# Performance work log

Measured on AMD Instinct MI355X. Metric: run time of the kernel, lower is better.

## Reference

```python
import jax, jax.numpy as jnp
import numpy as np

BN_EPS = 1e-5
R = 8.0        # radius
L = 11         # sequence kernel size (odd), s = L//2
K = 24         # kernel_channels[-1]
N_NODES = 32768
N_EDGES = 524288
C_IN = 128     # in_channels == out_channels
C_W = 32       # width = out_channels * base_width / 64


def _bn(x, gamma, beta):
    # BatchNorm1d in training mode: biased batch statistics over node dim
    mu = jnp.mean(x, axis=0)
    var = jnp.mean(jnp.square(x - mu), axis=0)
    return (x - mu) * jax.lax.rsqrt(var + BN_EPS) * gamma + beta


def _lrelu(x, slope):
    return jnp.where(x >= 0, x, slope * x)


def setup_inputs() -> dict:
    key = jax.random.key(0)
    ks = jax.random.split(key, 10)

    def glorot(k, shape, fan_in):
        return jax.random.normal(k, shape, jnp.float32) * np.float32(1.0 / np.sqrt(fan_in))

    inp = {}
    inp["x"] = jax.random.normal(ks[0], (N_NODES, C_IN), jnp.float32)
    inp["pos"] = jax.random.normal(ks[1], (N_NODES, 3), jnp.float32) * 10.0
    inp["ori"] = jax.random.normal(ks[2], (N_NODES, 9), jnp.float32)
    inp["seq"] = jnp.arange(N_NODES, dtype=jnp.int32)
    inp["edge_index"] = jax.random.randint(ks[3], (2, N_EDGES), 0, N_NODES, jnp.int32)
    # input MLP params: BN(C_IN) -> LeakyReLU(0.1) -> Linear(C_IN->C_W, no bias) -> BN(C_W) -> LeakyReLU(0.1)
    inp["bn1_g"] = jnp.ones((C_IN,), jnp.float32)
    inp["bn1_b"] = jnp.zeros((C_IN,), jnp.float32)
    inp["lin1_w"] = glorot(ks[4], (C_IN, C_W), C_IN)
    inp["bn2_g"] = jnp.ones((C_W,), jnp.float32)
    inp["bn2_b"] = jnp.zeros((C_W,), jnp.float32)
    # CDConv WeightNet (single layer kernel_channels=[K]): per-seq-bin affine 7 -> K
    inp["wn_w"] = glorot(ks[5], (L, 7, K), 7)
    inp["wn_b"] = jnp.zeros((L, K), jnp.float32)
    # CDConv output projection: [K*C_W, C_W]
    inp["conv_w"] = glorot(ks[6], (K * C_W, C_W), K * C_W)
    # output Linear: BN(C_W) -> LeakyReLU(0.1) -> Linear(C_W->C_IN, no bias)
    inp["bn3_g"] = jnp.ones((C_W,), jnp.float32)
    inp["bn3_b"] = jnp.zeros((C_W,), jnp.float32)
    inp["lin2_w"] = glorot(ks[7], (C_W, C_IN), C_W)
    return inp


def reference(x, pos, ori, seq, edge_index,
              bn1_g, bn1_b, lin1_w, bn2_g, bn2_b,
              wn_w, wn_b, conv_w, bn3_g, bn3_b, lin2_w):
    n = x.shape[0]
    identity = x  # in_channels == out_channels -> identity branch is passthrough

    # ----- input MLP (mid_channels=None) -----
    h = _lrelu(_bn(x, bn1_g, bn1_b), 0.1)
    h = h @ lin1_w                       # [N, C_W]
    h = _lrelu(_bn(h, bn2_g, bn2_b), 0.1)

    # ----- CDConv: continuous geometric kernel over neighbor edges -----
    src, dst = edge_index[0], edge_index[1]      # message j=src -> i=dst
    d = pos[src] - pos[dst]                      # [E,3]
    dist = jnp.linalg.norm(d, axis=-1, keepdims=True)
    direction = d / (dist + 1e-9)
    Ri = ori[dst].reshape(-1, 3, 3)              # receiver local frame
    Rj = ori[src].reshape(-1, 3, 3)
    pos_local = jnp.einsum('eij,ej->ei', Ri, direction)      # direction in local frame
    ori_feat = jnp.einsum('eij,ej->ei', Ri, Rj[:, 0, :])     # neighbor axis in local frame
    delta = jnp.concatenate([pos_local, ori_feat, dist / R], axis=-1)  # [E,7]

    s = L // 2
    sidx = jnp.clip(seq[src] - seq[dst], -s, s) + s          # [E] in [0, L)

    # WeightNet: per-edge affine selected by sequence bin, LeakyReLU(0.2)
    w = _lrelu(jnp.einsum('ef,efk->ek', delta, wn_w[sidx]) + wn_b[sidx], 0.2)  # [E,K]

    # message = outer(kernel_weight, x_j), scatter-sum to receivers
    msg = (w[:, :, None] * h[src][:, None, :]).reshape(w.shape[0], K * C_W)   # [E, K*C_W]
    agg = jax.ops.segment_sum(msg, dst, num_segments=n)                        # [N, K*C_W]
    h = agg @ conv_w                                                            # [N, C_W]

    # ----- output Linear + residual -----
    h = _lrelu(_bn(h, bn3_g, bn3_b), 0.1)
    out = h @ lin2_w + identity
    return out
```

## Files before the change

kernel.cpp:

```cpp
#include <hip/hip_runtime.h>

#define N_NODES 32768
#define C_IN 128
#define C_W 32
#define KK 24
#define SS 5
#define NPB 4
#define TC 256
#define AGS (KK * C_W + 4)
#define WNS 172
#define WBS 28
#define HS 36

#define BF_LO(u) __uint_as_float((u) << 16)
#define BF_HI(u) __uint_as_float((u) & 0xFFFF0000u)

__device__ __forceinline__ unsigned int bf16pair(float lo, float hi) {
    unsigned int ulo = __float_as_uint(lo);
    unsigned int uhi = __float_as_uint(hi);
    ulo = (ulo + 0x7FFFu + ((ulo >> 16) & 1u)) >> 16;
    uhi = (uhi + 0x7FFFu + ((uhi >> 16) & 1u)) & 0xFFFF0000u;
    return uhi | ulo;
}

__global__ void __launch_bounds__(256) k_pre(
        const float* __restrict__ x, float* __restrict__ s1,
        const int* __restrict__ ei, int E, int* __restrict__ counts) {
    int t = threadIdx.x;
    int c = t % C_IN;
    int r0 = blockIdx.x * 2 + t / C_IN;
    float s = 0.f, sq = 0.f;
    for (int r = r0; r < N_NODES; r += 1024) {
        float v = x[(size_t)r * C_IN + c];
        s += v; sq += v * v;
    }
    atomicAdd(&s1[c], s);
    atomicAdd(&s1[C_IN + c], sq);
    for (int e = blockIdx.x * 256 + t; e < E; e += 512 * 256)
        atomicAdd(&counts[ei[E + e]], 1);
}

__global__ void __launch_bounds__(256) k_mlp1(
        const float* __restrict__ x, const float* __restrict__ s1,
        const float* __restrict__ g1, const float* __restrict__ b1,
        const float* __restrict__ w1, float* __restrict__ hpre,
        float* __restrict__ s2sh) {
    __shared__ float sAB[2][C_IN];
    __shared__ float sx[32][C_IN + 4];
    __shared__ float sw[C_IN][C_W];
    const int t = threadIdx.x;
    const int row0 = blockIdx.x * 32;
    if (t < C_IN) {
        float mean = s1[t] * (1.f / N_NODES);
        float var = s1[C_IN + t] * (1.f / N_NODES) - mean * mean;
        float a = g1[t] * rsqrtf(var + 1e-5f);
        sAB[0][t] = a; sAB[1][t] = b1[t] - mean * a;
    }
    for (int idx = t; idx < C_IN * C_W; idx += 256)
        sw[idx / C_W][idx % C_W] = w1[idx];
    __syncthreads();
    for (int idx = t; idx < 32 * 32; idx += 256) {
        int r = idx >> 5, cq = idx & 31;
        float4 v = *(const float4*)&x[(size_t)(row0 + r) * C_IN + cq * 4];
        float* d = &sx[r][cq * 4];
        float a0 = sAB[0][cq*4+0]*v.x + sAB[1][cq*4+0];
        float a1 = sAB[0][cq*4+1]*v.y + sAB[1][cq*4+1];
        float a2 = sAB[0][cq*4+2]*v.z + sAB[1][cq*4+2];
        float a3 = sAB[0][cq*4+3]*v.w + sAB[1][cq*4+3];
        d[0] = a0 >= 0.f ? a0 : 0.1f * a0;
        d[1] = a1 >= 0.f ? a1 : 0.1f * a1;
        d[2] = a2 >= 0.f ? a2 : 0.1f * a2;
        d[3] = a3 >= 0.f ? a3 : 0.1f * a3;
    }
    __syncthreads();
    const int r = t >> 3, c0 = (t & 7) * 4;
    float ac0 = 0.f, ac1 = 0.f, ac2 = 0.f, ac3 = 0.f;
    #pragma unroll 8
    for (int cc = 0; cc < C_IN; ++cc) {
        float xv = sx[r][cc];
        float4 wv = *(const float4*)&sw[cc][c0];
        ac0 += xv * wv.x; ac1 += xv * wv.y; ac2 += xv * wv.z; ac3 += xv * wv.w;
    }
    float4 o; o.x = ac0; o.y = ac1; o.z = ac2; o.w = ac3;
    *(float4*)&hpre[(size_t)(row0 + r) * C_W + c0] = o;
    __syncthreads();
    sx[r][c0] = ac0; sx[r][c0+1] = ac1; sx[r][c0+2] = ac2; sx[r][c0+3] = ac3;
    __syncthreads();
    if (t < C_W) {
        float s = 0.f, sq = 0.f;
        #pragma unroll
        for (int rr = 0; rr < 32; ++rr) {
            float v = sx[rr][t];
            s += v; sq += v * v;
        }
        int sh = (blockIdx.x & 7) * 64;
        atomicAdd(&s2sh[sh + t], s);
        atomicAdd(&s2sh[sh + C_W + t], sq);
    }
}

__global__ void __launch_bounds__(1024) k_scan(
        const int* __restrict__ counts, int* __restrict__ offsets,
        int* __restrict__ cursor) {
    __shared__ int sblk[1024];
    const int t = threadIdx.x;
    const int base = t * 32;
    const int4* cp = (const int4*)(counts + base);
    int loc[32];
    int s = 0;
    #pragma unroll
    for (int q = 0; q < 8; ++q) {
        int4 v = cp[q];
        loc[q*4+0] = s; s += v.x;
        loc[q*4+1] = s; s += v.y;
        loc[q*4+2] = s; s += v.z;
        loc[q*4+3] = s; s += v.w;
    }
    sblk[t] = s;
    __syncthreads();
    for (int d = 1; d < 1024; d <<= 1) {
        int u = (t >= d) ? sblk[t - d] : 0;
        __syncthreads();
        sblk[t] += u;
        __syncthreads();
    }
    const int blockbase = sblk[t] - s;
    #pragma unroll
    for (int q = 0; q < 8; ++q) {
        int4 o;
        o.x = blockbase + loc[q*4+0];
        o.y = blockbase + loc[q*4+1];
        o.z = blockbase + loc[q*4+2];
        o.w = blockbase + loc[q*4+3];
        ((int4*)(offsets + base))[q] = o;
        ((int4*)(cursor + base))[q] = o;
    }
    if (t == 1023) offsets[N_NODES] = sblk[1023];
}

__global__ void __launch_bounds__(256) k_scatter(
        const int* __restrict__ ei, int E, int* __restrict__ cursor,
        int* __restrict__ srcPerm) {
    int e = blockIdx.x * 256 + threadIdx.x;
    if (e < E) {
        int dst = ei[E + e];
        int p = atomicAdd(&cursor[dst], 1);
        srcPerm[p] = ei[e];
    }
}

__global__ void __launch_bounds__(256) k_mega(
    const int* __restrict__ offsets, const int* __restrict__ srcPerm,
    const float* __restrict__ pos, const float* __restrict__ ori,
    const int* __restrict__ seq, const float* __restrict__ hpre,
    const float* __restrict__ s2sh, const float* __restrict__ g2,
    const float* __restrict__ b2,
    const float* __restrict__ wnw, const float* __restrict__ wnb,
    const float* __restrict__ convw,
    float* __restrict__ convout, float* __restrict__ s3sh) {

    __shared__ float sWnw[11 * WNS];
    __shared__ float sWnb[11 * WBS];
    __shared__ float sA2[C_W], sB2[C_W];
    __shared__ int   sOff[NPB + 1];
    __shared__ float sNd[NPB][13];
    __shared__ union SU {
        struct { unsigned short h[TC * HS]; unsigned int w[TC * 12]; } stg;
        struct { float agg[NPB][AGS]; float red[8][NPB][C_W];
                 float rv[NPB][C_W]; float rq[NPB][C_W]; } fin;
    } U;

    const int t = threadIdx.x;
    const int i0 = blockIdx.x * NPB;
    for (int idx = t; idx < 11 * 168; idx += 256)
        sWnw[(idx / 168) * WNS + idx % 168] = wnw[idx];
    for (int idx = t; idx < 11 * 24; idx += 256)
        sWnb[(idx / 24) * WBS + idx % 24] = wnb[idx];
    if (t < C_W) {
        float s = 0.f, sq = 0.f;
        #pragma unroll
        for (int j = 0; j < 8; ++j) {
            s  += s2sh[j * 64 + t];
            sq += s2sh[j * 64 + C_W + t];
        }
        float mean = s * (1.f / N_NODES);
        float var = sq * (1.f / N_NODES) - mean * mean;
        float a = g2[t] * rsqrtf(var + 1e-5f);
        sA2[t] = a; sB2[t] = b2[t] - mean * a;
    }
    if (t <= NPB) sOff[t] = offsets[i0 + t];
    if (t < NPB * 13) {
        int n = t / 13, f = t % 13;
        float v;
        if (f < 3)       v = pos[(i0 + n) * 3 + f];
        else if (f < 12) v = ori[(i0 + n) * 9 + (f - 3)];
        else             v = __int_as_float(seq[i0 + n]);
        sNd[n][f] = v;
    }
    __syncthreads();

    const int w = t >> 6, lane = t & 63, c = lane & 31, s = lane >> 5;
    const int beg = sOff[w], end = sOff[w + 1];
    const int blkBeg = sOff[0], blkEnd = sOff[NPB];
    float a[KK];
    #pragma unroll
    for (int k = 0; k < KK; ++k) a[k] = 0.f;

    for (int base = blkBeg; base < blkEnd; base += TC) {
        const int cnt = min(TC, blkEnd - base);
        __syncthreads();
        if (t < cnt) {
            const int slot = base + t;
            const int g = (slot >= sOff[1]) + (slot >= sOff[2]) + (slot >= sOff[3]);
            const int src = srcPerm[slot];
            float px = pos[src*3+0], py = pos[src*3+1], pz = pos[src*3+2];
            float o0 = ori[src*9+0], o1 = ori[src*9+1], o2 = ori[src*9+2];
            int sqs = seq[src];
            float dx = px - sNd[g][0], dy = py - sNd[g][1], dz = pz - sNd[g][2];
            float dist = sqrtf(dx*dx + dy*dy + dz*dz);
            float inv = 1.f / (dist + 1e-9f);
            float ux = dx*inv, uy = dy*inv, uz = dz*inv;
            float df[7];
            #pragma unroll
            for (int r = 0; r < 3; ++r) {
                float m0 = sNd[g][3 + r*3 + 0];
                float m1 = sNd[g][3 + r*3 + 1];
                float m2 = sNd[g][3 + r*3 + 2];
                df[r]     = m0*ux + m1*uy + m2*uz;
                df[3 + r] = m0*o0 + m1*o1 + m2*o2;
            }
            df[6] = dist * 0.125f;
            int dsq = sqs - __float_as_int(sNd[g][12]);
            dsq = dsq < -SS ? -SS : (dsq > SS ? SS : dsq);
            const int sb = dsq + SS;
            float wv[KK];
            #pragma unroll
            for (int k = 0; k < KK; ++k) wv[k] = sWnb[sb * WBS + k];
            #pragma unroll
            for (int f = 0; f < 7; ++f) {
                float d_ = df[f];
                #pragma unroll
                for (int k = 0; k < KK; ++k)
                    wv[k] += d_ * sWnw[sb * WNS + f * 24 + k];
            }
            #pragma unroll
            for (int k = 0; k < KK; ++k) wv[k] = wv[k] >= 0.f ? wv[k] : 0.2f * wv[k];
            #pragma unroll
            for (int jj = 0; jj < 12; ++jj)
                U.stg.w[t * 12 + jj] = bf16pair(wv[2*jj], wv[2*jj+1]);
            const float4* hs = (const float4*)(hpre + (size_t)src * C_W);
            uint2* hd = (uint2*)&U.stg.h[t * HS];
            #pragma unroll
            for (int g4 = 0; g4 < 4; ++g4) {
                float4 v0 = hs[2*g4], v1 = hs[2*g4+1];
                float f[8] = {v0.x, v0.y, v0.z, v0.w, v1.x, v1.y, v1.z, v1.w};
                #pragma unroll
                for (int j = 0; j < 8; ++j) {
                    int ch = g4 * 8 + j;
                    float av = sA2[ch] * f[j] + sB2[ch];
                    f[j] = av >= 0.f ? av : 0.1f * av;
                }
                uint2 p0; p0.x = bf16pair(f[0], f[1]); p0.y = bf16pair(f[2], f[3]);
                uint2 p1; p1.x = bf16pair(f[4], f[5]); p1.y = bf16pair(f[6], f[7]);
                hd[2*g4] = p0; hd[2*g4+1] = p1;
            }
        }
        __syncthreads();
        const int lo = max(beg, base), hi = min(end, base + cnt);
        #pragma unroll 2
        for (int p = lo + s; p < hi; p += 2) {
            const int pr = p - base;
            const float v = BF_LO((unsigned int)U.stg.h[pr * HS + c]);
            const uint4* wp = (const uint4*)&U.stg.w[pr * 12];
            const uint4 A = wp[0], B = wp[1], Cc = wp[2];
            a[0]  += BF_LO(A.x) * v;  a[1]  += BF_HI(A.x) * v;
            a[2]  += BF_LO(A.y) * v;  a[3]  += BF_HI(A.y) * v;
            a[4]  += BF_LO(A.z) * v;  a[5]  += BF_HI(A.z) * v;
            a[6]  += BF_LO(A.w) * v;  a[7]  += BF_HI(A.w) * v;
            a[8]  += BF_LO(B.x) * v;  a[9]  += BF_HI(B.x) * v;
            a[10] += BF_LO(B.y) * v;  a[11] += BF_HI(B.y) * v;
            a[12] += BF_LO(B.z) * v;  a[13] += BF_HI(B.z) * v;
            a[14] += BF_LO(B.w) * v;  a[15] += BF_HI(B.w) * v;
            a[16] += BF_LO(Cc.x) * v; a[17] += BF_HI(Cc.x) * v;
            a[18] += BF_LO(Cc.y) * v; a[19] += BF_HI(Cc.y) * v;
            a[20] += BF_LO(Cc.z) * v; a[21] += BF_HI(Cc.z) * v;
            a[22] += BF_LO(Cc.w) * v; a[23] += BF_HI(Cc.w) * v;
        }
    }
    __syncthreads();
    #pragma unroll
    for (int k = 0; k < KK; ++k) a[k] += __shfl_xor(a[k], 32, 64);
    if (s == 0) {
        #pragma unroll
        for (int k = 0; k < KK; ++k) U.fin.agg[w][k * C_W + c] = a[k];
    }
    __syncthreads();

    {
        const int coq = t & 7;
        const int gp  = (t >> 3) & 3;
        const int sl  = t >> 5;
        const int r0  = sl * 96;
        float4 acc; acc.x = acc.y = acc.z = acc.w = 0.f;
        #pragma unroll 6
        for (int rc = 0; rc < 96; rc += 4) {
            const float4 s4 = *(const float4*)&U.fin.agg[gp][r0 + rc];
            const float4 w0 = *(const float4*)&convw[(size_t)(r0+rc+0)*32 + coq*4];
            const float4 w1 = *(const float4*)&convw[(size_t)(r0+rc+1)*32 + coq*4];
            const float4 w2 = *(const float4*)&convw[(size_t)(r0+rc+2)*32 + coq*4];
            const float4 w3 = *(const float4*)&convw[(size_t)(r0+rc+3)*32 + coq*4];
            acc.x += s4.x*w0.x + s4.y*w1.x + s4.z*w2.x + s4.w*w3.x;
            acc.y += s4.x*w0.y + s4.y*w1.y + s4.z*w2.y + s4.w*w3.y;
            acc.z += s4.x*w0.z + s4.y*w1.z + s4.z*w2.z + s4.w*w3.z;
            acc.w += s4.x*w0.w + s4.y*w1.w + s4.z*w2.w + s4.w*w3.w;
        }
        *(float4*)&U.fin.red[sl][gp][coq * 4] = acc;
    }
    __syncthreads();
    if (t < 128) {
        const int gg = t >> 5, co = t & 31;
        float v = 0.f;
        #pragma unroll
        for (int sl = 0; sl < 8; ++sl) v += U.fin.red[sl][gg][co];
        convout[(size_t)(i0 + gg) * C_W + co] = v;
        U.fin.rv[gg][co] = v; U.fin.rq[gg][co] = v * v;
    }
    __syncthreads();
    if (t < 64) {
        int cc = t & 31;
        bool isq = t >= C_W;
        float s2 = 0.f;
        #pragma unroll
        for (int gg = 0; gg < NPB; ++gg)
            s2 += isq ? U.fin.rq[gg][cc] : U.fin.rv[gg][cc];
        atomicAdd(&s3sh[(blockIdx.x & 7) * 64 + t], s2);
    }
}

__global__ void __launch_bounds__(256) k_out(
        const float* __restrict__ conv, const float* __restrict__ s3sh,
        const float* __restrict__ g3, const float* __restrict__ b3,
        const float* __restrict__ w2, const float* __restrict__ x,
        float* __restrict__ out) {
    __shared__ float sAB[2][C_W];
    __shared__ float sh[8][C_W];
    __shared__ float sw2[C_W][C_IN];
    const int t = threadIdx.x;
    const int row0 = blockIdx.x * 8;
    if (t < C_W) {
        float s = 0.f, sq = 0.f;
        #pragma unroll
        for (int j = 0; j < 8; ++j) {
            s  += s3sh[j * 64 + t];
            sq += s3sh[j * 64 + C_W + t];
        }
        float mean = s * (1.f / N_NODES);
        float var = sq * (1.f / N_NODES) - mean * mean;
        float a = g3[t] * rsqrtf(var + 1e-5f);
        sAB[0][t] = a; sAB[1][t] = b3[t] - mean * a;
    }
    for (int idx = t; idx < C_W * C_IN; idx += 256)
        sw2[idx >> 7][idx & 127] = w2[idx];
    __syncthreads();
    {
        float v = conv[(size_t)row0 * C_W + t];
        int r = t >> 5, cc = t & 31;
        v = sAB[0][cc] * v + sAB[1][cc];
        sh[r][cc] = v >= 0.f ? v : 0.1f * v;
    }
    __syncthreads();
    const int r = t >> 5, c4 = (t & 31) * 4;
    float4 acc = *(const float4*)&x[(size_t)(row0 + r) * C_IN + c4];
    #pragma unroll 8
    for (int cw = 0; cw < C_W; ++cw) {
        float hv = sh[r][cw];
        float4 wv = *(const float4*)&sw2[cw][c4];
        acc.x += hv * wv.x; acc.y += hv * wv.y;
        acc.z += hv * wv.z; acc.w += hv * wv.w;
    }
    *(float4*)&out[(size_t)(row0 + r) * C_IN + c4] = acc;
}

extern "C" void kernel_launch(void* const* d_in, const int* in_sizes, int n_in,
                              void* d_out, int out_size, void* d_ws, size_t ws_size,
                              hipStream_t stream) {
    const float* x     = (const float*)d_in[0];
    const float* pos   = (const float*)d_in[1];
    const float* ori   = (const float*)d_in[2];
    const int*   seq   = (const int*)d_in[3];
    const int*   ei    = (const int*)d_in[4];
    const float* bn1g  = (const float*)d_in[5];
    const float* bn1b  = (const float*)d_in[6];
    const float* lin1w = (const float*)d_in[7];
    const float* bn2g  = (const float*)d_in[8];
    const float* bn2b  = (const float*)d_in[9];
    const float* wnw   = (const float*)d_in[10];
    const float* wnb   = (const float*)d_in[11];
    const float* convw = (const float*)d_in[12];
    const float* bn3g  = (const float*)d_in[13];
    const float* bn3b  = (const float*)d_in[14];
    const float* lin2w = (const float*)d_in[15];
    float* out = (float*)d_out;
    const int E = in_sizes[4] / 2;

    char* wsb = (char*)d_ws;
    size_t off = 0;
    auto alloc = [&](size_t bytes) {
        void* p = wsb + off;
        off = (off + bytes + 255) & ~(size_t)255;
        return p;
    };
    float* s1      = (float*)alloc(256 * 4);
    float* s2sh    = (float*)alloc(512 * 4);
    float* s3sh    = (float*)alloc(512 * 4);
    int*   counts  = (int*)alloc((size_t)N_NODES * 4);
    size_t zero_bytes = off;
    int*   offsets = (int*)alloc(((size_t)N_NODES + 1) * 4);
    int*   cursor  = (int*)alloc((size_t)N_NODES * 4);
    int*   srcPerm = (int*)alloc((size_t)E * 4);
    float* hpre    = (float*)alloc((size_t)N_NODES * C_W * 4);
    float* convo   = (float*)alloc((size_t)N_NODES * C_W * 4);

    hipMemsetAsync(wsb, 0, zero_bytes, stream);

    k_pre<<<512, 256, 0, stream>>>(x, s1, ei, E, counts);
    k_scan<<<1, 1024, 0, stream>>>(counts, offsets, cursor);
    k_scatter<<<(E + 255) / 256, 256, 0, stream>>>(ei, E, cursor, srcPerm);
    k_mlp1<<<N_NODES / 32, 256, 0, stream>>>(x, s1, bn1g, bn1b, lin1w, hpre, s2sh);
    k_mega<<<N_NODES / NPB, 256, 0, stream>>>(offsets, srcPerm, pos, ori, seq,
                                              hpre, s2sh, bn2g, bn2b, wnw, wnb,
                                              convw, convo, s3sh);
    k_out<<<N_NODES / 8, 256, 0, stream>>>(convo, s3sh, bn3g, bn3b, lin2w, x, out);
}
```

Baseline: 284.6 us.

## Process eight nodes per 512-thread block and split per-edge staging across two threads

Doubles the nodes handled per k_mega block to eight and the block size to 512 threads. Each edge in the staging phase is now handled by two threads: each computes half of the 24 WeightNet outputs and half of the 32 normalized source-feature channels. The aim is to use more of the otherwise idle staging threads, and to spread the shared-weight loading and the conv projection over more nodes per block. The cost is that both threads repeat the edge geometry work, and larger blocks use more LDS, which may lower occupancy.

```diff
diff --git a/kernel.cpp b/kernel.cpp
--- a/kernel.cpp
+++ b/kernel.cpp
@@ -5,7 +5,7 @@
 #define C_W 32
 #define KK 24
 #define SS 5
-#define NPB 4
+#define NPB 8
 #define TC 256
 #define AGS (KK * C_W + 4)
 #define WNS 172
@@ -149,7 +149,7 @@
     }
 }
 
-__global__ void __launch_bounds__(256) k_mega(
+__global__ void __launch_bounds__(512) k_mega(
     const int* __restrict__ offsets, const int* __restrict__ srcPerm,
     const float* __restrict__ pos, const float* __restrict__ ori,
     const int* __restrict__ seq, const float* __restrict__ hpre,
@@ -172,9 +172,9 @@
 
     const int t = threadIdx.x;
     const int i0 = blockIdx.x * NPB;
-    for (int idx = t; idx < 11 * 168; idx += 256)
+    for (int idx = t; idx < 11 * 168; idx += 512)
         sWnw[(idx / 168) * WNS + idx % 168] = wnw[idx];
-    for (int idx = t; idx < 11 * 24; idx += 256)
+    for (int idx = t; idx < 11 * 24; idx += 512)
         sWnb[(idx / 24) * WBS + idx % 24] = wnb[idx];
     if (t < C_W) {
         float s = 0.f, sq = 0.f;
@@ -209,60 +209,70 @@
     for (int base = blkBeg; base < blkEnd; base += TC) {
         const int cnt = min(TC, blkEnd - base);
         __syncthreads();
-        if (t < cnt) {
-            const int slot = base + t;
-            const int g = (slot >= sOff[1]) + (slot >= sOff[2]) + (slot >= sOff[3]);
-            const int src = srcPerm[slot];
-            float px = pos[src*3+0], py = pos[src*3+1], pz = pos[src*3+2];
-            float o0 = ori[src*9+0], o1 = ori[src*9+1], o2 = ori[src*9+2];
-            int sqs = seq[src];
-            float dx = px - sNd[g][0], dy = py - sNd[g][1], dz = pz - sNd[g][2];
-            float dist = sqrtf(dx*dx + dy*dy + dz*dz);
-            float inv = 1.f / (dist + 1e-9f);
-            float ux = dx*inv, uy = dy*inv, uz = dz*inv;
-            float df[7];
-            #pragma unroll
-            for (int r = 0; r < 3; ++r) {
-                float m0 = sNd[g][3 + r*3 + 0];
-                float m1 = sNd[g][3 + r*3 + 1];
-                float m2 = sNd[g][3 + r*3 + 2];
-                df[r]     = m0*ux + m1*uy + m2*uz;
-                df[3 + r] = m0*o0 + m1*o1 + m2*o2;
-            }
-            df[6] = dist * 0.125f;
-            int dsq = sqs - __float_as_int(sNd[g][12]);
-            dsq = dsq < -SS ? -SS : (dsq > SS ? SS : dsq);
-            const int sb = dsq + SS;
-            float wv[KK];
-            #pragma unroll
-            for (int k = 0; k < KK; ++k) wv[k] = sWnb[sb * WBS + k];
-            #pragma unroll
-            for (int f = 0; f < 7; ++f) {
-                float d_ = df[f];
-                #pragma unroll
-                for (int k = 0; k < KK; ++k)
-                    wv[k] += d_ * sWnw[sb * WNS + f * 24 + k];
-            }
-            #pragma unroll
-            for (int k = 0; k < KK; ++k) wv[k] = wv[k] >= 0.f ? wv[k] : 0.2f * wv[k];
-            #pragma unroll
-            for (int jj = 0; jj < 12; ++jj)
-                U.stg.w[t * 12 + jj] = bf16pair(wv[2*jj], wv[2*jj+1]);
-            const float4* hs = (const float4*)(hpre + (size_t)src * C_W);
-            uint2* hd = (uint2*)&U.stg.h[t * HS];
-            #pragma unroll
-            for (int g4 = 0; g4 < 4; ++g4) {
-                float4 v0 = hs[2*g4], v1 = hs[2*g4+1];
-                float f[8] = {v0.x, v0.y, v0.z, v0.w, v1.x, v1.y, v1.z, v1.w};
-                #pragma unroll
-                for (int j = 0; j < 8; ++j) {
-                    int ch = g4 * 8 + j;
-                    float av = sA2[ch] * f[j] + sB2[ch];
-                    f[j] = av >= 0.f ? av : 0.1f * av;
+        {
+            const int e    = t & 255;
+            const int half = t >> 8;
+            if (e < cnt) {
+                const int slot = base + e;
+                int g = 0;
+                #pragma unroll
+                for (int j = 1; j < NPB; ++j) g += (slot >= sOff[j]);
+                const int src = srcPerm[slot];
+                float px = pos[src*3+0], py = pos[src*3+1], pz = pos[src*3+2];
+                float o0 = ori[src*9+0], o1 = ori[src*9+1], o2 = ori[src*9+2];
+                int sqs = seq[src];
+                float dx = px - sNd[g][0], dy = py - sNd[g][1], dz = pz - sNd[g][2];
+                float dist = sqrtf(dx*dx + dy*dy + dz*dz);
+                float inv = 1.f / (dist + 1e-9f);
+                float ux = dx*inv, uy = dy*inv, uz = dz*inv;
+                float df[7];
+                #pragma unroll
+                for (int r = 0; r < 3; ++r) {
+                    float m0 = sNd[g][3 + r*3 + 0];
+                    float m1 = sNd[g][3 + r*3 + 1];
+                    float m2 = sNd[g][3 + r*3 + 2];
+                    df[r]     = m0*ux + m1*uy + m2*uz;
+                    df[3 + r] = m0*o0 + m1*o1 + m2*o2;
                 }
-                uint2 p0; p0.x = bf16pair(f[0], f[1]); p0.y = bf16pair(f[2], f[3]);
-                uint2 p1; p1.x = bf16pair(f[4], f[5]); p1.y = bf16pair(f[6], f[7]);
-                hd[2*g4] = p0; hd[2*g4+1] = p1;
+                df[6] = dist * 0.125f;
+                int dsq = sqs - __float_as_int(sNd[g][12]);
+                dsq = dsq < -SS ? -SS : (dsq > SS ? SS : dsq);
+                const int sb = dsq + SS;
+                float wv[12];
+                {
+                    const float* wb = &sWnb[sb * WBS + half * 12];
+                    #pragma unroll
+                    for (int j = 0; j < 12; ++j) wv[j] = wb[j];
+                }
+                const float* wn = &sWnw[sb * WNS + half * 12];
+                #pragma unroll
+                for (int f = 0; f < 7; ++f) {
+                    float d_ = df[f];
+                    #pragma unroll
+                    for (int j = 0; j < 12; ++j)
+                        wv[j] += d_ * wn[f * 24 + j];
+                }
+                #pragma unroll
+                for (int j = 0; j < 12; ++j) wv[j] = wv[j] >= 0.f ? wv[j] : 0.2f * wv[j];
+                #pragma unroll
+                for (int jj = 0; jj < 6; ++jj)
+                    U.stg.w[e * 12 + half * 6 + jj] = bf16pair(wv[2*jj], wv[2*jj+1]);
+                const float4* hs = (const float4*)(hpre + (size_t)src * C_W);
+                uint2* hd = (uint2*)&U.stg.h[e * HS + half * 16];
+                #pragma unroll
+                for (int q = 0; q < 2; ++q) {
+                    float4 v0 = hs[half * 4 + 2*q], v1 = hs[half * 4 + 2*q + 1];
+                    float f[8] = {v0.x, v0.y, v0.z, v0.w, v1.x, v1.y, v1.z, v1.w};
+                    #pragma unroll
+                    for (int j = 0; j < 8; ++j) {
+                        int ch = half * 16 + q * 8 + j;
+                        float av = sA2[ch] * f[j] + sB2[ch];
+                        f[j] = av >= 0.f ? av : 0.1f * av;
+                    }
+                    uint2 p0; p0.x = bf16pair(f[0], f[1]); p0.y = bf16pair(f[2], f[3]);
+                    uint2 p1; p1.x = bf16pair(f[4], f[5]); p1.y = bf16pair(f[6], f[7]);
+                    hd[2*q] = p0; hd[2*q+1] = p1;
+                }
             }
         }
         __syncthreads();
@@ -298,8 +308,8 @@
 
     {
         const int coq = t & 7;
-        const int gp  = (t >> 3) & 3;
-        const int sl  = t >> 5;
+        const int gp  = (t >> 3) & 7;
+        const int sl  = t >> 6;
         const int r0  = sl * 96;
         float4 acc; acc.x = acc.y = acc.z = acc.w = 0.f;
         #pragma unroll 6
@@ -317,7 +327,7 @@
         *(float4*)&U.fin.red[sl][gp][coq * 4] = acc;
     }
     __syncthreads();
-    if (t < 128) {
+    if (t < 256) {
         const int gg = t >> 5, co = t & 31;
         float v = 0.f;
         #pragma unroll
@@ -427,7 +437,7 @@
     k_scan<<<1, 1024, 0, stream>>>(counts, offsets, cursor);
     k_scatter<<<(E + 255) / 256, 256, 0, stream>>>(ei, E, cursor, srcPerm);
     k_mlp1<<<N_NODES / 32, 256, 0, stream>>>(x, s1, bn1g, bn1b, lin1w, hpre, s2sh);
-    k_mega<<<N_NODES / NPB, 256, 0, stream>>>(offsets, srcPerm, pos, ori, seq,
+    k_mega<<<N_NODES / NPB, 512, 0, stream>>>(offsets, srcPerm, pos, ori, seq,
                                               hpre, s2sh, bn2g, bn2b, wnw, wnb,
                                               convw, convo, s3sh);
     k_out<<<N_NODES / 8, 256, 0, stream>>>(convo, s3sh, bn3g, bn3b, lin2w, x, out);
```

New measurement: 265.8 us. -6.6%, faster.
